# Kernel tuning notes

Measured on AMD Instinct MI355X. Metric: run time of the kernel, lower is better.

The kernel has to match this reference:

```python
import jax, jax.numpy as jnp
import numpy as np
from jax import lax

HIDDEN = 10


def setup_inputs() -> dict:
    key = jax.random.key(0)
    ks = jax.random.split(key, 7)
    B, T, I, H, O = 4096, 512, 1, HIDDEN, 1
    return {
        "x": jax.random.normal(ks[0], (B, T, I), dtype=jnp.float32),
        "W_ih": jax.random.normal(ks[1], (4 * H, I), dtype=jnp.float32) * 0.3,
        "W_hh": jax.random.normal(ks[2], (4 * H, H), dtype=jnp.float32) * 0.3,
        "b_ih": jax.random.normal(ks[3], (4 * H,), dtype=jnp.float32) * 0.1,
        "b_hh": jax.random.normal(ks[4], (4 * H,), dtype=jnp.float32) * 0.1,
        "W_fc": jax.random.normal(ks[5], (O, H), dtype=jnp.float32) * 0.3,
        "b_fc": jax.random.normal(ks[6], (O,), dtype=jnp.float32) * 0.1,
    }


def reference(x, W_ih, W_hh, b_ih, b_hh, W_fc, b_fc):
    # x: [B, T, I]; single-layer LSTM (PyTorch gate order i, f, g, o), then
    # Linear on the last timestep's hidden state.
    B = x.shape[0]
    H = W_hh.shape[1]
    b = b_ih + b_hh  # fuse biases once

    def step(carry, xt):
        h, c = carry  # [B, H] each; xt: [B, I]
        gates = xt @ W_ih.T + h @ W_hh.T + b  # [B, 4H]
        i, f, g, o = jnp.split(gates, 4, axis=-1)
        i = jax.nn.sigmoid(i)
        f = jax.nn.sigmoid(f)
        g = jnp.tanh(g)
        o = jax.nn.sigmoid(o)
        c = f * c + i * g
        h = o * jnp.tanh(c)
        return (h, c), None

    h0 = jnp.zeros((B, H), dtype=x.dtype)
    c0 = jnp.zeros((B, H), dtype=x.dtype)
    x_tmajor = jnp.swapaxes(x, 0, 1)  # [T, B, I]
    (h_last, _), _ = lax.scan(step, (h0, c0), x_tmajor)
    return h_last @ W_fc.T + b_fc  # [B, O]
```

## Files before the change

kernel.cpp:

```cpp
#include <hip/hip_runtime.h>


#define NLOG2E (-1.4426950408889634f)

__device__ __forceinline__ float bperm(int byteaddr, float v) {
    return __int_as_float(__builtin_amdgcn_ds_bpermute(byteaddr, __float_as_int(v)));
}

__global__ __launch_bounds__(256, 1) void WeatherLSTM_kernel(
    const float* __restrict__ x,
    const float* __restrict__ W_ih,
    const float* __restrict__ W_hh,
    const float* __restrict__ b_ih,
    const float* __restrict__ b_hh,
    const float* __restrict__ W_fc,
    const float* __restrict__ b_fc,
    float* __restrict__ out,
    int T)
{
    const int tid  = threadIdx.x;
    const int lane = tid & 63;
    const int k    = tid & 15;
    const long e   = (long)blockIdx.x * 16 + (tid >> 4);
    const bool active = (k < 10);

    float whh[4][10], wih[4], bb[4];
    #pragma unroll
    for (int t = 0; t < 4; ++t) {
        const float s = (t == 2) ? (2.0f * NLOG2E) : NLOG2E;
        const int g = t * 10 + k;
        wih[t] = active ? W_ih[g] * s : 0.0f;
        bb[t]  = active ? (b_ih[g] + b_hh[g]) * s : 0.0f;
        #pragma unroll
        for (int j = 0; j < 10; ++j)
            whh[t][j] = active ? W_hh[g * 10 + j] * s : 0.0f;
    }

    float h[10];
    #pragma unroll
    for (int j = 0; j < 10; ++j) h[j] = 0.0f;
    float c = 0.0f, hown = 0.0f;

    const int base = (lane & 48) << 2;
    const float* xe = x + e * (long)T;

    for (int s0 = 0; s0 < T; s0 += 4) {
        const float4 xv = *reinterpret_cast<const float4*>(xe + s0);
        #pragma unroll
        for (int ss = 0; ss < 4; ++ss) {
            const float xt = (&xv.x)[ss];

            float a[4];
            #pragma unroll
            for (int t = 0; t < 4; ++t) {
                float accA = fmaf(xt, wih[t], bb[t]);
                float accB = h[5] * whh[t][5];
                #pragma unroll
                for (int j = 0; j < 5; ++j)
                    accA = fmaf(h[j], whh[t][j], accA);
                #pragma unroll
                for (int j = 6; j < 10; ++j)
                    accB = fmaf(h[j], whh[t][j], accB);
                const float acc = accA + accB;
                const float r = __builtin_amdgcn_rcpf(
                                    1.0f + __builtin_amdgcn_exp2f(acc));
                a[t] = (t == 2) ? fmaf(2.0f, r, -1.0f) : r;
            }

            c = fmaf(a[1], c, a[0] * a[2]);
            const float e2 = __builtin_amdgcn_exp2f(c * (2.0f * NLOG2E));
            hown = a[3] * fmaf(2.0f, __builtin_amdgcn_rcpf(1.0f + e2), -1.0f);

            #pragma unroll
            for (int j = 0; j < 10; ++j)
                h[j] = bperm(base + 4 * j, hown);
        }
    }

    if (k == 0) {
        float o = b_fc[0];
        #pragma unroll
        for (int j = 0; j < 10; ++j)
            o = fmaf(h[j], W_fc[j], o);
        out[e] = o;
    }
}

extern "C" void kernel_launch(void* const* d_in, const int* in_sizes, int n_in,
                              void* d_out, int out_size, void* d_ws, size_t ws_size,
                              hipStream_t stream) {
    const float* x    = (const float*)d_in[0];
    const float* W_ih = (const float*)d_in[1];
    const float* W_hh = (const float*)d_in[2];
    const float* b_ih = (const float*)d_in[3];
    const float* b_hh = (const float*)d_in[4];
    const float* W_fc = (const float*)d_in[5];
    const float* b_fc = (const float*)d_in[6];
    float* out = (float*)d_out;

    const int B = out_size;
    const int T = in_sizes[0] / B;

    dim3 grid(B / 16), block(256);
    hipLaunchKernelGGL(WeatherLSTM_kernel, grid, block, 0, stream,
                       x, W_ih, W_hh, b_ih, b_hh, W_fc, b_fc, out, T);
}
```

Baseline: 104.6 us.

## Split LSTM gates across wave halves with permlane32 swap and LDS broadcast

Each batch element now spans two 16-lane groups in different wave halves, and each half computes two of the four gates. Gate values are exchanged with permlane32_swap, and the hidden state is broadcast through shared memory instead of ten ds_bpermute calls per step. The grid doubles to B/8 blocks, launch bounds allow 2 blocks per CU, and the x load is software-prefetched one float4 ahead. The goal is to halve the serial FMA and transcendental chain per step and add parallelism, at the cost of twice as many threads and an LDS write/read round trip each step, which relies on wave-synchronous execution without explicit barriers.

After: 109.1 us (median of 2 runs). 4.3% more time.

```diff
diff --git a/kernel.cpp b/kernel.cpp
--- a/kernel.cpp
+++ b/kernel.cpp
@@ -3,11 +3,78 @@
 
 #define NLOG2E (-1.4426950408889634f)
 
-__device__ __forceinline__ float bperm(int byteaddr, float v) {
-    return __int_as_float(__builtin_amdgcn_ds_bpermute(byteaddr, __float_as_int(v)));
+template<bool PICKX>
+__device__ __forceinline__ float pickf(unsigned x, unsigned y) {
+    return __uint_as_float(PICKX ? x : y);
 }
 
-__global__ __launch_bounds__(256, 1) void WeatherLSTM_kernel(
+template<bool PICKX>
+__device__ __forceinline__ void lstm_run(
+    const float* __restrict__ xe, int T,
+    const float (&wh)[2][10], float wi0, float wi1, float bb0, float bb1,
+    float fm, float fa, float* hrow, float (&h)[10])
+{
+    const int k = threadIdx.x & 15;
+    #pragma unroll
+    for (int j = 0; j < 10; ++j) h[j] = 0.0f;
+    float c = 0.0f;
+
+    float4 xv = *reinterpret_cast<const float4*>(xe);
+    for (int s0 = 0; s0 < T; s0 += 4) {
+        const int snext = (s0 + 4 < T) ? (s0 + 4) : s0;
+        const float4 xnext = *reinterpret_cast<const float4*>(xe + snext);
+        #pragma unroll
+        for (int ss = 0; ss < 4; ++ss) {
+            const float xt = (&xv.x)[ss];
+
+            float aA0 = fmaf(xt, wi0, bb0);
+            float aA1 = fmaf(xt, wi1, bb1);
+            float aB0 = h[5] * wh[0][5];
+            float aB1 = h[5] * wh[1][5];
+            #pragma unroll
+            for (int j = 0; j < 5; ++j) {
+                aA0 = fmaf(h[j], wh[0][j], aA0);
+                aA1 = fmaf(h[j], wh[1][j], aA1);
+            }
+            #pragma unroll
+            for (int j = 6; j < 10; ++j) {
+                aB0 = fmaf(h[j], wh[0][j], aB0);
+                aB1 = fmaf(h[j], wh[1][j], aB1);
+            }
+            const float r0 = __builtin_amdgcn_rcpf(
+                1.0f + __builtin_amdgcn_exp2f(aA0 + aB0));
+            const float r1 = __builtin_amdgcn_rcpf(
+                1.0f + __builtin_amdgcn_exp2f(aA1 + aB1));
+            const float a0 = fmaf(fm, r0, fa);
+            const float a1 = r1;
+
+            auto w0 = __builtin_amdgcn_permlane32_swap(
+                __float_as_uint(a0), __float_as_uint(a0), false, false);
+            auto w1 = __builtin_amdgcn_permlane32_swap(
+                __float_as_uint(a1), __float_as_uint(a1), false, false);
+            const float iv = pickf<PICKX>(w0[0], w0[1]);
+            const float gv = pickf<PICKX>(w0[1], w0[0]);
+            const float fv = pickf<PICKX>(w1[0], w1[1]);
+            const float ov = pickf<PICKX>(w1[1], w1[0]);
+
+            c = fmaf(fv, c, iv * gv);
+            const float e2 = __builtin_amdgcn_exp2f(c * (2.0f * NLOG2E));
+            const float th = fmaf(2.0f, __builtin_amdgcn_rcpf(1.0f + e2), -1.0f);
+            const float hown = ov * th;
+
+            hrow[k] = hown;
+            const float4 h03 = *reinterpret_cast<const float4*>(hrow);
+            const float4 h47 = *reinterpret_cast<const float4*>(hrow + 4);
+            const float2 h89 = *reinterpret_cast<const float2*>(hrow + 8);
+            h[0] = h03.x; h[1] = h03.y; h[2] = h03.z; h[3] = h03.w;
+            h[4] = h47.x; h[5] = h47.y; h[6] = h47.z; h[7] = h47.w;
+            h[8] = h89.x; h[9] = h89.y;
+        }
+        xv = xnext;
+    }
+}
+
+__global__ __launch_bounds__(256, 2) void WeatherLSTM_kernel(
     const float* __restrict__ x,
     const float* __restrict__ W_ih,
     const float* __restrict__ W_hh,
@@ -18,66 +85,44 @@
     float* __restrict__ out,
     int T)
 {
+    __shared__ float hsh[8][16];
     const int tid  = threadIdx.x;
     const int lane = tid & 63;
-    const int k    = tid & 15;
-    const long e   = (long)blockIdx.x * 16 + (tid >> 4);
-    const bool active = (k < 10);
+    const int wav  = tid >> 6;
+    const int k    = lane & 15;
+    const int h1   = lane >> 5;
+    const int eib  = wav * 2 + ((lane >> 4) & 1);
+    const long e   = (long)blockIdx.x * 8 + eib;
+    const bool act = (k < 10);
 
-    float whh[4][10], wih[4], bb[4];
+    float wh[2][10], wiv[2], bbv[2];
     #pragma unroll
-    for (int t = 0; t < 4; ++t) {
+    for (int p = 0; p < 2; ++p) {
+        const int t = 2 * h1 + p;
         const float s = (t == 2) ? (2.0f * NLOG2E) : NLOG2E;
         const int g = t * 10 + k;
-        wih[t] = active ? W_ih[g] * s : 0.0f;
-        bb[t]  = active ? (b_ih[g] + b_hh[g]) * s : 0.0f;
+        wiv[p] = act ? W_ih[g] * s : 0.0f;
+        bbv[p] = act ? (b_ih[g] + b_hh[g]) * s : 0.0f;
         #pragma unroll
         for (int j = 0; j < 10; ++j)
-            whh[t][j] = active ? W_hh[g * 10 + j] * s : 0.0f;
+            wh[p][j] = act ? W_hh[g * 10 + j] * s : 0.0f;
     }
+    const float fm = h1 ? 2.0f : 1.0f;
+    const float fa = h1 ? -1.0f : 0.0f;
+
+    auto pr = __builtin_amdgcn_permlane32_swap((unsigned)lane, (unsigned)lane,
+                                               false, false);
+    const bool pickx = ((int)pr[0] == (lane & 31));
 
     float h[10];
-    #pragma unroll
-    for (int j = 0; j < 10; ++j) h[j] = 0.0f;
-    float c = 0.0f, hown = 0.0f;
+    if (pickx)
+        lstm_run<true >(x + e * (long)T, T, wh, wiv[0], wiv[1], bbv[0], bbv[1],
+                        fm, fa, &hsh[eib][0], h);
+    else
+        lstm_run<false>(x + e * (long)T, T, wh, wiv[0], wiv[1], bbv[0], bbv[1],
+                        fm, fa, &hsh[eib][0], h);
 
-    const int base = (lane & 48) << 2;
-    const float* xe = x + e * (long)T;
-
-    for (int s0 = 0; s0 < T; s0 += 4) {
-        const float4 xv = *reinterpret_cast<const float4*>(xe + s0);
-        #pragma unroll
-        for (int ss = 0; ss < 4; ++ss) {
-            const float xt = (&xv.x)[ss];
-
-            float a[4];
-            #pragma unroll
-            for (int t = 0; t < 4; ++t) {
-                float accA = fmaf(xt, wih[t], bb[t]);
-                float accB = h[5] * whh[t][5];
-                #pragma unroll
-                for (int j = 0; j < 5; ++j)
-                    accA = fmaf(h[j], whh[t][j], accA);
-                #pragma unroll
-                for (int j = 6; j < 10; ++j)
-                    accB = fmaf(h[j], whh[t][j], accB);
-                const float acc = accA + accB;
-                const float r = __builtin_amdgcn_rcpf(
-                                    1.0f + __builtin_amdgcn_exp2f(acc));
-                a[t] = (t == 2) ? fmaf(2.0f, r, -1.0f) : r;
-            }
-
-            c = fmaf(a[1], c, a[0] * a[2]);
-            const float e2 = __builtin_amdgcn_exp2f(c * (2.0f * NLOG2E));
-            hown = a[3] * fmaf(2.0f, __builtin_amdgcn_rcpf(1.0f + e2), -1.0f);
-
-            #pragma unroll
-            for (int j = 0; j < 10; ++j)
-                h[j] = bperm(base + 4 * j, hown);
-        }
-    }
-
-    if (k == 0) {
+    if (k == 0 && h1 == 0) {
         float o = b_fc[0];
         #pragma unroll
         for (int j = 0; j < 10; ++j)
@@ -101,7 +146,7 @@
     const int B = out_size;
     const int T = in_sizes[0] / B;
 
-    dim3 grid(B / 16), block(256);
+    dim3 grid(B / 8), block(256);
     hipLaunchKernelGGL(WeatherLSTM_kernel, grid, block, 0, stream,
                        x, W_ih, W_hh, b_ih, b_hh, W_fc, b_fc, out, T);
 }
```

## Pack gate FMAs with v_pk_fma_f32, broadcast h via LDS, fuse sigmoid reciprocals

Applied to the files above, without the earlier changes.

Gate weights are regrouped into (i,f) and (g,o) pairs so the recurrent matvec runs on packed v_pk_fma_f32 instructions, halving the FMA count per step. The sigmoid and tanh reciprocals are combined algebraically, so each step issues fewer rcp instructions. The hidden state is shared through a small LDS row with five 128-bit reads instead of ten ds_bpermute calls. The next x chunk is also prefetched one iteration ahead. The LDS exchange has no barrier and relies on each 16-lane group sitting inside one wavefront, and the packed layout raises register use.

After: 92.44 us. -11.6%, faster.

```diff
diff --git a/kernel.cpp b/kernel.cpp
--- a/kernel.cpp
+++ b/kernel.cpp
@@ -3,8 +3,23 @@
 
 #define NLOG2E (-1.4426950408889634f)
 
-__device__ __forceinline__ float bperm(int byteaddr, float v) {
-    return __int_as_float(__builtin_amdgcn_ds_bpermute(byteaddr, __float_as_int(v)));
+typedef float f2 __attribute__((ext_vector_type(2)));
+typedef float f4 __attribute__((ext_vector_type(4)));
+
+__device__ __forceinline__ f2 pk_fma(f2 a, f2 b, f2 c) {
+    f2 d;
+    asm("v_pk_fma_f32 %0, %1, %2, %3" : "=v"(d) : "v"(a), "v"(b), "v"(c));
+    return d;
+}
+__device__ __forceinline__ f2 pk_mul(f2 a, f2 b) {
+    f2 d;
+    asm("v_pk_mul_f32 %0, %1, %2" : "=v"(d) : "v"(a), "v"(b));
+    return d;
+}
+__device__ __forceinline__ f2 pk_add(f2 a, f2 b) {
+    f2 d;
+    asm("v_pk_add_f32 %0, %1, %2" : "=v"(d) : "v"(a), "v"(b));
+    return d;
 }
 
 __global__ __launch_bounds__(256, 1) void WeatherLSTM_kernel(
@@ -18,70 +33,94 @@
     float* __restrict__ out,
     int T)
 {
-    const int tid  = threadIdx.x;
-    const int lane = tid & 63;
-    const int k    = tid & 15;
-    const long e   = (long)blockIdx.x * 16 + (tid >> 4);
-    const bool active = (k < 10);
+    __shared__ float hsh[16][24];
+    const int tid = threadIdx.x;
+    const int k   = tid & 15;
+    const int kw  = (k < 10) ? k : 10;
+    const int grp = tid >> 4;
+    const long e  = (long)blockIdx.x * 16 + grp;
+    const bool act = (k < 10);
+    float* hrow = &hsh[grp][0];
 
-    float whh[4][10], wih[4], bb[4];
-    #pragma unroll
-    for (int t = 0; t < 4; ++t) {
-        const float s = (t == 2) ? (2.0f * NLOG2E) : NLOG2E;
-        const int g = t * 10 + k;
-        wih[t] = active ? W_ih[g] * s : 0.0f;
-        bb[t]  = active ? (b_ih[g] + b_hh[g]) * s : 0.0f;
+    const float sI = NLOG2E, sF = NLOG2E, sG = 2.0f * NLOG2E, sO = NLOG2E;
+    f2 wIF[10], wGO[10], xwIF, xwGO, bIF, bGO;
+    {
+        const int gi = 0 * 10 + k, gf = 1 * 10 + k, gg = 2 * 10 + k, go = 3 * 10 + k;
+        xwIF = act ? f2{W_ih[gi] * sI, W_ih[gf] * sF} : f2{0.f, 0.f};
+        xwGO = act ? f2{W_ih[gg] * sG, W_ih[go] * sO} : f2{0.f, 0.f};
+        bIF  = act ? f2{(b_ih[gi] + b_hh[gi]) * sI, (b_ih[gf] + b_hh[gf]) * sF}
+                   : f2{0.f, 0.f};
+        bGO  = act ? f2{(b_ih[gg] + b_hh[gg]) * sG, (b_ih[go] + b_hh[go]) * sO}
+                   : f2{0.f, 0.f};
         #pragma unroll
-        for (int j = 0; j < 10; ++j)
-            whh[t][j] = active ? W_hh[g * 10 + j] * s : 0.0f;
+        for (int j = 0; j < 10; ++j) {
+            wIF[j] = act ? f2{W_hh[gi * 10 + j] * sI, W_hh[gf * 10 + j] * sF}
+                         : f2{0.f, 0.f};
+            wGO[j] = act ? f2{W_hh[gg * 10 + j] * sG, W_hh[go * 10 + j] * sO}
+                         : f2{0.f, 0.f};
+        }
     }
 
-    float h[10];
+    f2 h2[10];
     #pragma unroll
-    for (int j = 0; j < 10; ++j) h[j] = 0.0f;
-    float c = 0.0f, hown = 0.0f;
+    for (int j = 0; j < 10; ++j) h2[j] = f2{0.f, 0.f};
+    float c = 0.0f;
 
-    const int base = (lane & 48) << 2;
     const float* xe = x + e * (long)T;
-
+    f4 xv = *reinterpret_cast<const f4*>(xe);
     for (int s0 = 0; s0 < T; s0 += 4) {
-        const float4 xv = *reinterpret_cast<const float4*>(xe + s0);
+        const int snext = (s0 + 4 < T) ? (s0 + 4) : s0;
+        const f4 xnext = *reinterpret_cast<const f4*>(xe + snext);
         #pragma unroll
         for (int ss = 0; ss < 4; ++ss) {
-            const float xt = (&xv.x)[ss];
+            const float xt = xv[ss];
+            const f2 xt2 = f2{xt, xt};
 
-            float a[4];
+            f2 aIF0 = pk_fma(xt2, xwIF, bIF);
+            f2 aGO0 = pk_fma(xt2, xwGO, bGO);
+            f2 aIF1 = pk_mul(h2[5], wIF[5]);
+            f2 aGO1 = pk_mul(h2[5], wGO[5]);
             #pragma unroll
-            for (int t = 0; t < 4; ++t) {
-                float accA = fmaf(xt, wih[t], bb[t]);
-                float accB = h[5] * whh[t][5];
-                #pragma unroll
-                for (int j = 0; j < 5; ++j)
-                    accA = fmaf(h[j], whh[t][j], accA);
-                #pragma unroll
-                for (int j = 6; j < 10; ++j)
-                    accB = fmaf(h[j], whh[t][j], accB);
-                const float acc = accA + accB;
-                const float r = __builtin_amdgcn_rcpf(
-                                    1.0f + __builtin_amdgcn_exp2f(acc));
-                a[t] = (t == 2) ? fmaf(2.0f, r, -1.0f) : r;
+            for (int j = 0; j < 5; ++j) {
+                aIF0 = pk_fma(h2[j], wIF[j], aIF0);
+                aGO0 = pk_fma(h2[j], wGO[j], aGO0);
             }
+            #pragma unroll
+            for (int j = 6; j < 10; ++j) {
+                aIF1 = pk_fma(h2[j], wIF[j], aIF1);
+                aGO1 = pk_fma(h2[j], wGO[j], aGO1);
+            }
+            const f2 aIF = pk_add(aIF0, aIF1);
+            const f2 aGO = pk_add(aGO0, aGO1);
 
-            c = fmaf(a[1], c, a[0] * a[2]);
-            const float e2 = __builtin_amdgcn_exp2f(c * (2.0f * NLOG2E));
-            hown = a[3] * fmaf(2.0f, __builtin_amdgcn_rcpf(1.0f + e2), -1.0f);
+            const float pi = __builtin_amdgcn_exp2f(aIF[0]);
+            const float pf = __builtin_amdgcn_exp2f(aIF[1]);
+            const float pg = __builtin_amdgcn_exp2f(aGO[0]);
+            const float po = __builtin_amdgcn_exp2f(aGO[1]);
+            const float f  = __builtin_amdgcn_rcpf(1.0f + pf);
+            const float ig = (1.0f - pg) *
+                __builtin_amdgcn_rcpf((1.0f + pi) * (1.0f + pg));
+            c = fmaf(f, c, ig);
+            const float pc = __builtin_amdgcn_exp2f(c * (2.0f * NLOG2E));
+            const float hown = (1.0f - pc) *
+                __builtin_amdgcn_rcpf((1.0f + po) * (1.0f + pc));
 
+            *reinterpret_cast<f2*>(hrow + 2 * kw) = f2{hown, hown};
             #pragma unroll
-            for (int j = 0; j < 10; ++j)
-                h[j] = bperm(base + 4 * j, hown);
+            for (int r = 0; r < 5; ++r) {
+                const f4 v = *reinterpret_cast<const f4*>(hrow + 4 * r);
+                h2[2 * r]     = f2{v[0], v[1]};
+                h2[2 * r + 1] = f2{v[2], v[3]};
+            }
         }
+        xv = xnext;
     }
 
     if (k == 0) {
         float o = b_fc[0];
         #pragma unroll
         for (int j = 0; j < 10; ++j)
-            o = fmaf(h[j], W_fc[j], o);
+            o = fmaf(h2[j][0], W_fc[j], o);
         out[e] = o;
     }
 }
```

## Merge gate reciprocals algebraically, interleave gate FMAs, and prefetch next x chunk

Applied to the files above, without the earlier changes.

The gate activations are rewritten so the sigmoid and tanh reciprocals collapse into two rcp calls per step instead of five, combining the cell update into one fraction. The gate dot-product loops are reordered so the four gates' FMA chains interleave, which exposes instruction-level parallelism along the serial recurrence. The next float4 of x is loaded one chunk ahead to hide global load latency. The combined products could overflow or lose precision when exponentials grow large, which would produce inf/NaN where the per-gate form stayed bounded.

Result: faster. 102.2 us (-2.4%).

```diff
diff --git a/kernel.cpp b/kernel.cpp
--- a/kernel.cpp
+++ b/kernel.cpp
@@ -2,6 +2,8 @@
 
 
 #define NLOG2E (-1.4426950408889634f)
+
+typedef float f4 __attribute__((ext_vector_type(4)));
 
 __device__ __forceinline__ float bperm(int byteaddr, float v) {
     return __int_as_float(__builtin_amdgcn_ds_bpermute(byteaddr, __float_as_int(v)));
@@ -21,60 +23,76 @@
     const int tid  = threadIdx.x;
     const int lane = tid & 63;
     const int k    = tid & 15;
-    const long e   = (long)blockIdx.x * 16 + (tid >> 4);
-    const bool active = (k < 10);
+    const int grp  = tid >> 4;
+    const long e   = (long)blockIdx.x * 16 + grp;
+    const bool act = (k < 10);
 
-    float whh[4][10], wih[4], bb[4];
+    float wh[4][10], wx[4], bb[4];
     #pragma unroll
     for (int t = 0; t < 4; ++t) {
         const float s = (t == 2) ? (2.0f * NLOG2E) : NLOG2E;
         const int g = t * 10 + k;
-        wih[t] = active ? W_ih[g] * s : 0.0f;
-        bb[t]  = active ? (b_ih[g] + b_hh[g]) * s : 0.0f;
+        wx[t] = act ? W_ih[g] * s : 0.0f;
+        bb[t] = act ? (b_ih[g] + b_hh[g]) * s : 0.0f;
         #pragma unroll
         for (int j = 0; j < 10; ++j)
-            whh[t][j] = active ? W_hh[g * 10 + j] * s : 0.0f;
+            wh[t][j] = act ? W_hh[g * 10 + j] * s : 0.0f;
     }
+
+    const int base = (lane & 48) << 2;
 
     float h[10];
     #pragma unroll
     for (int j = 0; j < 10; ++j) h[j] = 0.0f;
     float c = 0.0f, hown = 0.0f;
 
-    const int base = (lane & 48) << 2;
     const float* xe = x + e * (long)T;
-
+    f4 xv = *reinterpret_cast<const f4*>(xe);
     for (int s0 = 0; s0 < T; s0 += 4) {
-        const float4 xv = *reinterpret_cast<const float4*>(xe + s0);
+        const int snext = (s0 + 4 < T) ? (s0 + 4) : s0;
+        const f4 xnext = *reinterpret_cast<const f4*>(xe + snext);
         #pragma unroll
         for (int ss = 0; ss < 4; ++ss) {
-            const float xt = (&xv.x)[ss];
+            const float xt = xv[ss];
 
-            float a[4];
+            float accA[4], accB[4];
             #pragma unroll
             for (int t = 0; t < 4; ++t) {
-                float accA = fmaf(xt, wih[t], bb[t]);
-                float accB = h[5] * whh[t][5];
+                accA[t] = fmaf(xt, wx[t], bb[t]);
+                accB[t] = h[5] * wh[t][5];
+            }
+            #pragma unroll
+            for (int j = 0; j < 5; ++j) {
                 #pragma unroll
-                for (int j = 0; j < 5; ++j)
-                    accA = fmaf(h[j], whh[t][j], accA);
+                for (int t = 0; t < 4; ++t)
+                    accA[t] = fmaf(h[j], wh[t][j], accA[t]);
+            }
+            #pragma unroll
+            for (int j = 6; j < 10; ++j) {
                 #pragma unroll
-                for (int j = 6; j < 10; ++j)
-                    accB = fmaf(h[j], whh[t][j], accB);
-                const float acc = accA + accB;
-                const float r = __builtin_amdgcn_rcpf(
-                                    1.0f + __builtin_amdgcn_exp2f(acc));
-                a[t] = (t == 2) ? fmaf(2.0f, r, -1.0f) : r;
+                for (int t = 0; t < 4; ++t)
+                    accB[t] = fmaf(h[j], wh[t][j], accB[t]);
             }
+            const float pi = __builtin_amdgcn_exp2f(accA[0] + accB[0]);
+            const float pf = __builtin_amdgcn_exp2f(accA[1] + accB[1]);
+            const float pg = __builtin_amdgcn_exp2f(accA[2] + accB[2]);
+            const float po = __builtin_amdgcn_exp2f(accA[3] + accB[3]);
 
-            c = fmaf(a[1], c, a[0] * a[2]);
-            const float e2 = __builtin_amdgcn_exp2f(c * (2.0f * NLOG2E));
-            hown = a[3] * fmaf(2.0f, __builtin_amdgcn_rcpf(1.0f + e2), -1.0f);
+            const float qi = 1.0f + pi, qf = 1.0f + pf, qg = 1.0f + pg;
+            const float mg = 1.0f - pg;
+            const float A   = qi * qg;
+            const float num = fmaf(c, A, mg * qf);
+            c = num * __builtin_amdgcn_rcpf(A * qf);
+
+            const float pc = __builtin_amdgcn_exp2f(c * (2.0f * NLOG2E));
+            const float qo = 1.0f + po, qc = 1.0f + pc, mc = 1.0f - pc;
+            hown = mc * __builtin_amdgcn_rcpf(qo * qc);
 
             #pragma unroll
             for (int j = 0; j < 10; ++j)
                 h[j] = bperm(base + 4 * j, hown);
         }
+        xv = xnext;
     }
 
     if (k == 0) {
```
